# Performance work log

Measured on AMD Instinct MI355X. Metric: run time of the kernel, lower is better.

The kernel has to match this reference:

```python
import jax, jax.numpy as jnp
import numpy as np
import math

SQ, SK, B, NP, HN = 2048, 2048, 2, 16, 128
LAYER_NUM = 1  # coeff
NORM_FACTOR = math.sqrt(2048 / 16) * LAYER_NUM  # sqrt(HIDDEN/HEADS) * coeff
SCALE = float(LAYER_NUM)  # MLSASoftmax scale


def setup_inputs() -> dict:
    key = jax.random.key(0)
    kq, kk, kv = jax.random.split(key, 3)
    query_layer = jax.random.normal(kq, (SQ, B, NP, HN), dtype=jnp.float32)
    key_layer = jax.random.normal(kk, (SK, B, NP, HN), dtype=jnp.float32)
    value_layer = jax.random.normal(kv, (SK, B, NP, HN), dtype=jnp.float32)
    # Causal mask: True = masked, shape [b, 1, sq, sk] (broadcasts over heads)
    causal = jnp.triu(jnp.ones((SQ, SK), dtype=bool), k=1)
    attention_mask = jnp.broadcast_to(causal[None, None], (B, 1, SQ, SK))
    return {
        "query_layer": query_layer,
        "key_layer": key_layer,
        "value_layer": value_layer,
        "attention_mask": attention_mask,
    }


def reference(query_layer, key_layer, value_layer, attention_mask):
    # scores[b,n,s,t] = (Q . K) / norm_factor, then * coeff in softmax
    scores = jnp.einsum("sbnh,tbnh->bnst", query_layer, key_layer) / NORM_FACTOR
    scores = scores * SCALE
    scores = jnp.where(attention_mask, jnp.float32(-10000.0), scores)
    # Module computes exp/sum WITHOUT max-subtraction; replicate exactly.
    exp_mo = jnp.exp(scores)
    denomi = jnp.sum(exp_mo, axis=-1, keepdims=True)  # [b, np, sq, 1]
    probs = exp_mo / denomi
    # dropout is identity in eval / for deterministic baseline
    ctx = jnp.einsum("bnst,tbnh->sbnh", probs, value_layer)  # [sq, b, np, hn]
    sq, b, n, h = ctx.shape
    context_layer = ctx.reshape(sq, b, n * h)
    return (context_layer, denomi)
```

## Files before the change

### kernel.cpp

```cpp
#include <hip/hip_runtime.h>
#include <hip/hip_bf16.h>
#include <stdint.h>

typedef __attribute__((ext_vector_type(8))) short short8;
typedef __attribute__((ext_vector_type(8))) unsigned short ushort8;
typedef __attribute__((ext_vector_type(4))) float f32x4;
typedef __attribute__((ext_vector_type(4))) int int4v;

#define NHEAD 32
#define SEQ   2048
#define HN    128

static constexpr float INV_NORM = 0.08838834764831845f;

__device__ __forceinline__ unsigned short f2bf(float f) {
  union { float f; unsigned u; } v; v.f = f;
  unsigned r = v.u + 0x7fffu + ((v.u >> 16) & 1u);
  return (unsigned short)(r >> 16);
}

__device__ __forceinline__ f32x4 mfma16(short8 a, short8 b, f32x4 c) {
  return __builtin_amdgcn_mfma_f32_16x16x32_bf16(a, b, c, 0, 0, 0);
}

__device__ __forceinline__ void gl_lds16(const void* g, void* l) {
  __builtin_amdgcn_global_load_lds(
      (const __attribute__((address_space(1))) unsigned int*)g,
      (__attribute__((address_space(3))) unsigned int*)l, 16, 0, 0);
}

__global__ __launch_bounds__(256) void prep_kv(const float* __restrict__ K,
                                               const float* __restrict__ V,
                                               unsigned short* __restrict__ kswz,
                                               unsigned short* __restrict__ vT) {
  __shared__ unsigned short lds[128 * 136];
  int bid = blockIdx.x;
  int tid = threadIdx.x;
  if (bid < 4096) {
    int idx = bid * 256 + tid;
    int cl = idx & 15;
    int t  = (idx >> 4) & 2047;
    int bn = idx >> 15;
    const float4* src = (const float4*)(K + ((size_t)t * 32 + bn) * 128 + cl * 8);
    float4 a = src[0], b = src[1];
    ushort8 o;
    o[0]=f2bf(a.x); o[1]=f2bf(a.y); o[2]=f2bf(a.z); o[3]=f2bf(a.w);
    o[4]=f2bf(b.x); o[5]=f2bf(b.y); o[6]=f2bf(b.z); o[7]=f2bf(b.w);
    *(ushort8*)(kswz + ((size_t)bn * 2048 + t) * 128 + ((cl ^ (t & 7)) * 8)) = o;
  } else {
    int vb = bid - 4096;
    int bn = vb >> 4;
    int t0 = (vb & 15) << 7;
    int r = tid >> 1, h0 = (tid & 1) * 64;
    const float* src = V + ((size_t)(t0 + r) * 32 + bn) * 128 + h0;
#pragma unroll
    for (int j = 0; j < 8; ++j) {
      float4 a = *(const float4*)(src + j * 8);
      float4 b = *(const float4*)(src + j * 8 + 4);
      ushort8 o;
      o[0]=f2bf(a.x); o[1]=f2bf(a.y); o[2]=f2bf(a.z); o[3]=f2bf(a.w);
      o[4]=f2bf(b.x); o[5]=f2bf(b.y); o[6]=f2bf(b.z); o[7]=f2bf(b.w);
      *(ushort8*)&lds[r * 136 + h0 + j * 8] = o;
    }
    __syncthreads();
    int h = tid >> 1, ts = (tid & 1) * 64;
    unsigned short tmp[64];
#pragma unroll
    for (int j = 0; j < 64; ++j) {
      int p = j & 31;
      int tloc = ((p >> 3) & 3) * 4 + ((p >> 2) & 1) * 16 + (p & 3);
      tmp[j] = lds[(ts + (j & 32) + tloc) * 136 + h];
    }
    ushort8* dst = (ushort8*)(vT + ((size_t)bn * 128 + h) * 2048 + t0 + ts);
#pragma unroll
    for (int j = 0; j < 8; ++j) dst[j] = *(ushort8*)&tmp[j * 8];
  }
}

__device__ __forceinline__ void read_kf(const char* kb, int l15, int hi,
                                        short8 (&kf)[2][4]) {
  int xr = (l15 & 7) << 4;
#pragma unroll
  for (int nt = 0; nt < 2; ++nt) {
    const char* krow = kb + (nt * 16 + l15) * 256;
#pragma unroll
    for (int kk = 0; kk < 4; ++kk)
      kf[nt][kk] = *(const short8*)(krow + (((kk * 4 + hi) * 16) ^ xr));
  }
}

__device__ __forceinline__ void read_vf(const char* vbh, int l15, int hi,
                                        short8 (&vf)[8]) {
#pragma unroll
  for (int ht = 0; ht < 8; ++ht)
    vf[ht] = *(const short8*)(vbh + (ht * 16 + l15) * 64 +
                              ((((l15 >> 1) + hi) & 3) * 16));
}

__device__ __forceinline__ short8 packp(const float (&e)[8], float& da) {
  da += ((e[0] + e[1]) + (e[2] + e[3])) + ((e[4] + e[5]) + (e[6] + e[7]));
  unsigned w0, w1, w2, w3;
  asm("v_cvt_pk_bf16_f32 %0, %1, %2" : "=v"(w0) : "v"(e[0]), "v"(e[1]));
  asm("v_cvt_pk_bf16_f32 %0, %1, %2" : "=v"(w1) : "v"(e[2]), "v"(e[3]));
  asm("v_cvt_pk_bf16_f32 %0, %1, %2" : "=v"(w2) : "v"(e[4]), "v"(e[5]));
  asm("v_cvt_pk_bf16_f32 %0, %1, %2" : "=v"(w3) : "v"(e[6]), "v"(e[7]));
  union { int4v u; short8 s; } pk;
  pk.u = (int4v){(int)w0, (int)w1, (int)w2, (int)w3};
  return pk.s;
}

__device__ __forceinline__ short8 softp_m(const f32x4 (&sv)[2], int t0h, int qbase,
                                          int l15, int hi, float& da) {
  float e[8];
#pragma unroll
  for (int nt = 0; nt < 2; ++nt)
#pragma unroll
    for (int i = 0; i < 4; ++i) {
      float x = __expf(sv[nt][i]);
      int kv = t0h + nt * 16 + hi * 4 + i;
      e[nt * 4 + i] = (kv <= qbase + l15) ? x : 0.0f;
    }
  return packp(e, da);
}

__device__ __forceinline__ short8 softp_u(const f32x4 (&sv)[2], float& da) {
  float e[8];
#pragma unroll
  for (int nt = 0; nt < 2; ++nt)
#pragma unroll
    for (int i = 0; i < 4; ++i)
      e[nt * 4 + i] = __expf(sv[nt][i]);
  return packp(e, da);
}

__global__ __launch_bounds__(256, 2) void attn_main(const float* __restrict__ Q,
                                                    const unsigned short* __restrict__ kswz,
                                                    const unsigned short* __restrict__ vT,
                                                    float* __restrict__ out) {
  __shared__ char smem[32768];
  int tid = threadIdx.x;
  int lane = tid & 63;
  int w = tid >> 6;
  int l15 = lane & 15;
  int hi = lane >> 4;

  int bid = blockIdx.x;
  int bn = bid & 31;
  int z = bid >> 5;
  int g = z & 7, s = z >> 3;
  int qt = (s == 0) ? (31 - g) : (s == 1) ? (16 + g) : (s == 2) ? (15 - g) : g;
  int qb = qt * 64 + w * 16;
  int ntile = 2 * qt + 2;

  short8 qf[4];
  {
    const float* qrow = Q + ((size_t)(qb + l15) * 32 + bn) * 128;
#pragma unroll
    for (int kk = 0; kk < 4; ++kk) {
      float4 a = *(const float4*)(qrow + kk * 32 + hi * 8);
      float4 b = *(const float4*)(qrow + kk * 32 + hi * 8 + 4);
      short8 o;
      o[0]=(short)f2bf(a.x*INV_NORM); o[1]=(short)f2bf(a.y*INV_NORM);
      o[2]=(short)f2bf(a.z*INV_NORM); o[3]=(short)f2bf(a.w*INV_NORM);
      o[4]=(short)f2bf(b.x*INV_NORM); o[5]=(short)f2bf(b.y*INV_NORM);
      o[6]=(short)f2bf(b.z*INV_NORM); o[7]=(short)f2bf(b.w*INV_NORM);
      qf[kk] = o;
    }
  }

  f32x4 zz = {0.f, 0.f, 0.f, 0.f};
  f32x4 acc[8];
#pragma unroll
  for (int ht = 0; ht < 8; ++ht) acc[ht] = zz;
  float dacc = 0.f;

  const char* kg = (const char*)(kswz + (size_t)bn * 2048 * 128);
  const char* vg = (const char*)(vT + (size_t)bn * 128 * 2048);

  auto stage = [&](int buf, int t) {
    const char* ksrc = kg + (size_t)t * 8192;
    char* kl = smem + buf * 8192;
    int c = w * 64 + lane;
#pragma unroll
    for (int rr = 0; rr < 2; ++rr)
      gl_lds16(ksrc + (size_t)(c + rr * 256) * 16, kl + (c + rr * 256) * 16);
    char* vl = smem + 16384 + buf * 8192;
#pragma unroll
    for (int rr = 0; rr < 2; ++rr) {
      int c2 = c + rr * 256;
      int h = c2 >> 2, sp = c2 & 3;
      int sl = (sp - (h >> 1)) & 3;
      gl_lds16(vg + (size_t)h * 4096 + (size_t)t * 64 + sl * 16,
               vl + c2 * 16);
    }
  };

  asm volatile("s_waitcnt vmcnt(0)" ::: "memory");
  stage(0, 0);

  int cur = 0;
  for (int it = 0; it < ntile; ++it) {
    int t0h = it * 32;
    asm volatile("s_waitcnt vmcnt(0)" ::: "memory");
    __builtin_amdgcn_s_barrier();

    const char* kb = smem + cur * 8192;
    const char* vbh = smem + 16384 + cur * 8192;
    bool act = (t0h <= qb + 15);

    short8 kf[2][4];
    if (act) read_kf(kb, l15, hi, kf);
    if (it + 1 < ntile) stage(cur ^ 1, it + 1);

    if (act) {
      f32x4 sv[2] = {zz, zz};
      __builtin_amdgcn_s_setprio(1);
#pragma unroll
      for (int nt = 0; nt < 2; ++nt)
#pragma unroll
        for (int kk = 0; kk < 4; ++kk)
          sv[nt] = mfma16(kf[nt][kk], qf[kk], sv[nt]);
      __builtin_amdgcn_s_setprio(0);
      short8 vf[8];
      read_vf(vbh, l15, hi, vf);
      bool mask = (t0h + 31 > qb);
      short8 p = mask ? softp_m(sv, t0h, qb, l15, hi, dacc)
                      : softp_u(sv, dacc);
      __builtin_amdgcn_s_setprio(1);
#pragma unroll
      for (int ht = 0; ht < 8; ++ht)
        acc[ht] = mfma16(p, vf[ht], acc[ht]);
      __builtin_amdgcn_s_setprio(0);
    }
    cur ^= 1;
  }

  {
    float d = dacc;
    d += __shfl_xor(d, 16);
    d += __shfl_xor(d, 32);
    dacc = d;
  }
  float* dn = out + 8388608;
  if (hi == 0) dn[(size_t)bn * 2048 + qb + l15] = dacc;

  float inv[4];
#pragma unroll
  for (int i = 0; i < 4; ++i)
    inv[i] = __builtin_amdgcn_rcpf(__shfl(dacc, hi * 4 + i));

#pragma unroll
  for (int i = 0; i < 4; ++i) {
    float* orow = out + (size_t)(qb + hi * 4 + i) * 4096 + bn * 128 + l15;
#pragma unroll
    for (int ht = 0; ht < 8; ++ht)
      orow[ht * 16] = acc[ht][i] * inv[i];
  }
}

extern "C" void kernel_launch(void* const* d_in, const int* in_sizes, int n_in,
                              void* d_out, int out_size, void* d_ws, size_t ws_size,
                              hipStream_t stream) {
  const float* Q = (const float*)d_in[0];
  const float* K = (const float*)d_in[1];
  const float* V = (const float*)d_in[2];
  float* out = (float*)d_out;

  unsigned short* kswz = (unsigned short*)d_ws;
  unsigned short* vT   = kswz + (size_t)NHEAD * SEQ * HN;

  prep_kv<<<4608, 256, 0, stream>>>(K, V, kswz, vT);
  attn_main<<<1024, 256, 0, stream>>>(Q, kswz, vT, out);
}
```

Baseline: 85.30 us.

## Split KV loop across two wave groups per block and merge partial results

Doubles the block to 512 threads. Two groups of four waves each process alternating KV tiles with their own double-buffered LDS regions, then merge the partial accumulators and denominators through shared memory. The aim is to halve the serial KV loop length per block and expose more parallelism for the causal workload. The q-tile ordering is simplified to descending order. The cost is double the LDS (64KB), a shared-memory reduction epilogue, and likely lower occupancy.

```diff
diff --git a/kernel.cpp b/kernel.cpp
--- a/kernel.cpp
+++ b/kernel.cpp
@@ -133,24 +133,25 @@
   return packp(e, da);
 }
 
-__global__ __launch_bounds__(256, 2) void attn_main(const float* __restrict__ Q,
+__global__ __launch_bounds__(512, 2) void attn_main(const float* __restrict__ Q,
                                                     const unsigned short* __restrict__ kswz,
                                                     const unsigned short* __restrict__ vT,
                                                     float* __restrict__ out) {
-  __shared__ char smem[32768];
+  __shared__ char smem[65536];
   int tid = threadIdx.x;
   int lane = tid & 63;
-  int w = tid >> 6;
+  int w8 = tid >> 6;
+  int w = w8 & 3;
+  int sid = w8 >> 2;
   int l15 = lane & 15;
   int hi = lane >> 4;
 
   int bid = blockIdx.x;
   int bn = bid & 31;
   int z = bid >> 5;
-  int g = z & 7, s = z >> 3;
-  int qt = (s == 0) ? (31 - g) : (s == 1) ? (16 + g) : (s == 2) ? (15 - g) : g;
+  int qt = 31 - z;
   int qb = qt * 64 + w * 16;
-  int ntile = 2 * qt + 2;
+  int nIt = qt + 1;
 
   short8 qf[4];
   {
@@ -177,14 +178,17 @@
   const char* kg = (const char*)(kswz + (size_t)bn * 2048 * 128);
   const char* vg = (const char*)(vT + (size_t)bn * 128 * 2048);
 
+  char* kbase = smem + sid * 16384;
+  char* vbase = smem + 32768 + sid * 16384;
+
   auto stage = [&](int buf, int t) {
     const char* ksrc = kg + (size_t)t * 8192;
-    char* kl = smem + buf * 8192;
+    char* kl = kbase + buf * 8192;
     int c = w * 64 + lane;
 #pragma unroll
     for (int rr = 0; rr < 2; ++rr)
       gl_lds16(ksrc + (size_t)(c + rr * 256) * 16, kl + (c + rr * 256) * 16);
-    char* vl = smem + 16384 + buf * 8192;
+    char* vl = vbase + buf * 8192;
 #pragma unroll
     for (int rr = 0; rr < 2; ++rr) {
       int c2 = c + rr * 256;
@@ -196,21 +200,22 @@
   };
 
   asm volatile("s_waitcnt vmcnt(0)" ::: "memory");
-  stage(0, 0);
+  stage(0, sid);
 
   int cur = 0;
-  for (int it = 0; it < ntile; ++it) {
-    int t0h = it * 32;
+  for (int it = 0; it < nIt; ++it) {
+    int t = it * 2 + sid;
+    int t0h = t * 32;
     asm volatile("s_waitcnt vmcnt(0)" ::: "memory");
     __builtin_amdgcn_s_barrier();
 
-    const char* kb = smem + cur * 8192;
-    const char* vbh = smem + 16384 + cur * 8192;
+    const char* kb = kbase + cur * 8192;
+    const char* vbh = vbase + cur * 8192;
     bool act = (t0h <= qb + 15);
 
     short8 kf[2][4];
     if (act) read_kf(kb, l15, hi, kf);
-    if (it + 1 < ntile) stage(cur ^ 1, it + 1);
+    if (it + 1 < nIt) stage(cur ^ 1, t + 2);
 
     if (act) {
       f32x4 sv[2] = {zz, zz};
@@ -235,6 +240,27 @@
     cur ^= 1;
   }
 
+  __syncthreads();
+  int sl = w * 64 + lane;
+  float* dsm = (float*)smem;
+  if (sid == 1) dsm[sl] = dacc;
+  __syncthreads();
+  if (sid == 0) dacc += dsm[sl];
+  __syncthreads();
+  f32x4* accsm = (f32x4*)smem;
+  if (sid == 1) {
+#pragma unroll
+    for (int ht = 0; ht < 8; ++ht) accsm[ht * 256 + sl] = acc[ht];
+  }
+  __syncthreads();
+  if (sid == 1) return;
+#pragma unroll
+  for (int ht = 0; ht < 8; ++ht) {
+    f32x4 o = accsm[ht * 256 + sl];
+    acc[ht][0] += o[0]; acc[ht][1] += o[1];
+    acc[ht][2] += o[2]; acc[ht][3] += o[3];
+  }
+
   {
     float d = dacc;
     d += __shfl_xor(d, 16);
@@ -270,5 +296,5 @@
   unsigned short* vT   = kswz + (size_t)NHEAD * SEQ * HN;
 
   prep_kv<<<4608, 256, 0, stream>>>(K, V, kswz, vT);
-  attn_main<<<1024, 256, 0, stream>>>(Q, kswz, vT, out);
-}
+  attn_main<<<1024, 512, 0, stream>>>(Q, kswz, vT, out);
+}
```

New measurement: 93.65 us. 1.1x slower.

## Double block size to 8 waves and 128-row query tiles with 64-key stages

Applied to the files above, without the earlier changes.

Each block now runs 8 waves covering 128 query rows and stages 64 keys per iteration (two 32-key halves) into a doubled 64KB LDS double buffer. Each staged K/V tile is shared by twice as many waves, which halves global-to-LDS traffic per query and halves the number of barriers. The block schedule is simplified to a 16-tile reverse/forward ordering. In exchange the grid drops to 512 blocks, LDS use per block doubles, and causal load balancing is coarser because inactive waves still wait at each barrier.

```diff
diff --git a/kernel.cpp b/kernel.cpp
--- a/kernel.cpp
+++ b/kernel.cpp
@@ -133,11 +133,11 @@
   return packp(e, da);
 }
 
-__global__ __launch_bounds__(256, 2) void attn_main(const float* __restrict__ Q,
+__global__ __launch_bounds__(512, 2) void attn_main(const float* __restrict__ Q,
                                                     const unsigned short* __restrict__ kswz,
                                                     const unsigned short* __restrict__ vT,
                                                     float* __restrict__ out) {
-  __shared__ char smem[32768];
+  __shared__ char smem[65536];
   int tid = threadIdx.x;
   int lane = tid & 63;
   int w = tid >> 6;
@@ -147,9 +147,8 @@
   int bid = blockIdx.x;
   int bn = bid & 31;
   int z = bid >> 5;
-  int g = z & 7, s = z >> 3;
-  int qt = (s == 0) ? (31 - g) : (s == 1) ? (16 + g) : (s == 2) ? (15 - g) : g;
-  int qb = qt * 64 + w * 16;
+  int qt = (z < 8) ? (15 - z) : (z - 8);
+  int qb = qt * 128 + w * 16;
   int ntile = 2 * qt + 2;
 
   short8 qf[4];
@@ -177,21 +176,20 @@
   const char* kg = (const char*)(kswz + (size_t)bn * 2048 * 128);
   const char* vg = (const char*)(vT + (size_t)bn * 128 * 2048);
 
-  auto stage = [&](int buf, int t) {
-    const char* ksrc = kg + (size_t)t * 8192;
-    char* kl = smem + buf * 8192;
-    int c = w * 64 + lane;
+  auto stage = [&](int buf, int t0) {
+    const char* ksrc = kg + (size_t)t0 * 256;
+    char* kl = smem + buf * 16384;
+    int c = tid;
 #pragma unroll
     for (int rr = 0; rr < 2; ++rr)
-      gl_lds16(ksrc + (size_t)(c + rr * 256) * 16, kl + (c + rr * 256) * 16);
-    char* vl = smem + 16384 + buf * 8192;
-#pragma unroll
-    for (int rr = 0; rr < 2; ++rr) {
-      int c2 = c + rr * 256;
-      int h = c2 >> 2, sp = c2 & 3;
+      gl_lds16(ksrc + (size_t)(c + rr * 512) * 16, kl + (c + rr * 512) * 16);
+    char* vl = smem + 32768 + buf * 16384;
+#pragma unroll
+    for (int s = 0; s < 2; ++s) {
+      int h = c >> 2, sp = c & 3;
       int sl = (sp - (h >> 1)) & 3;
-      gl_lds16(vg + (size_t)h * 4096 + (size_t)t * 64 + sl * 16,
-               vl + c2 * 16);
+      gl_lds16(vg + (size_t)h * 4096 + (t0 + s * 32) * 2 + sl * 16,
+               vl + s * 8192 + c * 16);
     }
   };
 
@@ -200,37 +198,40 @@
 
   int cur = 0;
   for (int it = 0; it < ntile; ++it) {
-    int t0h = it * 32;
+    int t0 = it * 64;
     asm volatile("s_waitcnt vmcnt(0)" ::: "memory");
     __builtin_amdgcn_s_barrier();
-
-    const char* kb = smem + cur * 8192;
-    const char* vbh = smem + 16384 + cur * 8192;
-    bool act = (t0h <= qb + 15);
-
-    short8 kf[2][4];
-    if (act) read_kf(kb, l15, hi, kf);
-    if (it + 1 < ntile) stage(cur ^ 1, it + 1);
-
-    if (act) {
-      f32x4 sv[2] = {zz, zz};
-      __builtin_amdgcn_s_setprio(1);
-#pragma unroll
-      for (int nt = 0; nt < 2; ++nt)
-#pragma unroll
-        for (int kk = 0; kk < 4; ++kk)
-          sv[nt] = mfma16(kf[nt][kk], qf[kk], sv[nt]);
-      __builtin_amdgcn_s_setprio(0);
-      short8 vf[8];
-      read_vf(vbh, l15, hi, vf);
-      bool mask = (t0h + 31 > qb);
-      short8 p = mask ? softp_m(sv, t0h, qb, l15, hi, dacc)
-                      : softp_u(sv, dacc);
-      __builtin_amdgcn_s_setprio(1);
-#pragma unroll
-      for (int ht = 0; ht < 8; ++ht)
-        acc[ht] = mfma16(p, vf[ht], acc[ht]);
-      __builtin_amdgcn_s_setprio(0);
+    if (it + 1 < ntile) stage(cur ^ 1, t0 + 64);
+
+    const char* kb = smem + cur * 16384;
+    const char* vb = smem + 32768 + cur * 16384;
+#pragma unroll
+    for (int half = 0; half < 2; ++half) {
+      int t0h = t0 + half * 32;
+      if (t0h <= qb + 15) {
+        const char* kbh = kb + half * 8192;
+        const char* vbh = vb + half * 8192;
+        short8 kf[2][4];
+        read_kf(kbh, l15, hi, kf);
+        f32x4 sv[2] = {zz, zz};
+        __builtin_amdgcn_s_setprio(1);
+#pragma unroll
+        for (int nt = 0; nt < 2; ++nt)
+#pragma unroll
+          for (int kk = 0; kk < 4; ++kk)
+            sv[nt] = mfma16(kf[nt][kk], qf[kk], sv[nt]);
+        __builtin_amdgcn_s_setprio(0);
+        short8 vf[8];
+        read_vf(vbh, l15, hi, vf);
+        bool mask = (t0h + 31 > qb);
+        short8 p = mask ? softp_m(sv, t0h, qb, l15, hi, dacc)
+                        : softp_u(sv, dacc);
+        __builtin_amdgcn_s_setprio(1);
+#pragma unroll
+        for (int ht = 0; ht < 8; ++ht)
+          acc[ht] = mfma16(p, vf[ht], acc[ht]);
+        __builtin_amdgcn_s_setprio(0);
+      }
     }
     cur ^= 1;
   }
@@ -270,5 +271,5 @@
   unsigned short* vT   = kswz + (size_t)NHEAD * SEQ * HN;
 
   prep_kv<<<4608, 256, 0, stream>>>(K, V, kswz, vT);
-  attn_main<<<1024, 256, 0, stream>>>(Q, kswz, vT, out);
-}
+  attn_main<<<512, 512, 0, stream>>>(Q, kswz, vT, out);
+}
```

Measured after the change: 80.74 us. 5.3% less time.

## Pre-layout K/V in MFMA fragment order and load directly from global, dropping LDS staging

Applied to the files above, without the earlier changes.

The prep kernel now writes K and V in the exact per-lane MFMA fragment order, so the attention kernel can read each fragment with a coalesced 16-byte global load per lane. This removes the LDS double buffer, the global-to-LDS copies and the per-tile barriers, and lets each wave exit its loop independently once its causal range ends. The query-tile scheduling order is also changed. In exchange, K/V are re-read from L2 by every wave with no software prefetch, so memory latency is exposed more directly.

```diff
diff --git a/kernel.cpp b/kernel.cpp
--- a/kernel.cpp
+++ b/kernel.cpp
@@ -23,16 +23,10 @@
   return __builtin_amdgcn_mfma_f32_16x16x32_bf16(a, b, c, 0, 0, 0);
 }
 
-__device__ __forceinline__ void gl_lds16(const void* g, void* l) {
-  __builtin_amdgcn_global_load_lds(
-      (const __attribute__((address_space(1))) unsigned int*)g,
-      (__attribute__((address_space(3))) unsigned int*)l, 16, 0, 0);
-}
-
 __global__ __launch_bounds__(256) void prep_kv(const float* __restrict__ K,
                                                const float* __restrict__ V,
-                                               unsigned short* __restrict__ kswz,
-                                               unsigned short* __restrict__ vT) {
+                                               unsigned short* __restrict__ kfr,
+                                               unsigned short* __restrict__ vfr) {
   __shared__ unsigned short lds[128 * 136];
   int bid = blockIdx.x;
   int tid = threadIdx.x;
@@ -46,7 +40,11 @@
     ushort8 o;
     o[0]=f2bf(a.x); o[1]=f2bf(a.y); o[2]=f2bf(a.z); o[3]=f2bf(a.w);
     o[4]=f2bf(b.x); o[5]=f2bf(b.y); o[6]=f2bf(b.z); o[7]=f2bf(b.w);
-    *(ushort8*)(kswz + ((size_t)bn * 2048 + t) * 128 + ((cl ^ (t & 7)) * 8)) = o;
+    int tile = t >> 5, r = t & 31;
+    int nt = r >> 4, lr = r & 15;
+    int kk = cl >> 2, hc = cl & 3;
+    *(ushort8*)(kfr + (size_t)bn * 262144 + tile * 4096 +
+                (nt * 4 + kk) * 512 + (hc * 16 + lr) * 8) = o;
   } else {
     int vb = bid - 4096;
     int bn = vb >> 4;
@@ -71,30 +69,16 @@
       int tloc = ((p >> 3) & 3) * 4 + ((p >> 2) & 1) * 16 + (p & 3);
       tmp[j] = lds[(ts + (j & 32) + tloc) * 136 + h];
     }
-    ushort8* dst = (ushort8*)(vT + ((size_t)bn * 128 + h) * 2048 + t0 + ts);
-#pragma unroll
-    for (int j = 0; j < 8; ++j) dst[j] = *(ushort8*)&tmp[j * 8];
-  }
-}
-
-__device__ __forceinline__ void read_kf(const char* kb, int l15, int hi,
-                                        short8 (&kf)[2][4]) {
-  int xr = (l15 & 7) << 4;
-#pragma unroll
-  for (int nt = 0; nt < 2; ++nt) {
-    const char* krow = kb + (nt * 16 + l15) * 256;
-#pragma unroll
-    for (int kk = 0; kk < 4; ++kk)
-      kf[nt][kk] = *(const short8*)(krow + (((kk * 4 + hi) * 16) ^ xr));
-  }
-}
-
-__device__ __forceinline__ void read_vf(const char* vbh, int l15, int hi,
-                                        short8 (&vf)[8]) {
-#pragma unroll
-  for (int ht = 0; ht < 8; ++ht)
-    vf[ht] = *(const short8*)(vbh + (ht * 16 + l15) * 64 +
-                              ((((l15 >> 1) + hi) & 3) * 16));
+#pragma unroll
+    for (int j = 0; j < 8; ++j) {
+      int c0 = t0 + ts + j * 8;
+      int tg = c0 >> 5;
+      int hv = (c0 >> 3) & 3;
+      size_t du = (size_t)bn * 32768 + (size_t)tg * 512 +
+                  (h >> 4) * 64 + hv * 16 + (h & 15);
+      *(ushort8*)(vfr + du * 8) = *(ushort8*)&tmp[j * 8];
+    }
+  }
 }
 
 __device__ __forceinline__ short8 packp(const float (&e)[8], float& da) {
@@ -134,10 +118,9 @@
 }
 
 __global__ __launch_bounds__(256, 2) void attn_main(const float* __restrict__ Q,
-                                                    const unsigned short* __restrict__ kswz,
-                                                    const unsigned short* __restrict__ vT,
+                                                    const unsigned short* __restrict__ kfr,
+                                                    const unsigned short* __restrict__ vfr,
                                                     float* __restrict__ out) {
-  __shared__ char smem[32768];
   int tid = threadIdx.x;
   int lane = tid & 63;
   int w = tid >> 6;
@@ -147,8 +130,8 @@
   int bid = blockIdx.x;
   int bn = bid & 31;
   int z = bid >> 5;
-  int g = z & 7, s = z >> 3;
-  int qt = (s == 0) ? (31 - g) : (s == 1) ? (16 + g) : (s == 2) ? (15 - g) : g;
+  int qt = (z < 8) ? (31 - z) : (z < 16) ? (z - 8)
+                   : (z < 24) ? (39 - z) : (z - 16);
   int qb = qt * 64 + w * 16;
   int ntile = 2 * qt + 2;
 
@@ -174,65 +157,45 @@
   for (int ht = 0; ht < 8; ++ht) acc[ht] = zz;
   float dacc = 0.f;
 
-  const char* kg = (const char*)(kswz + (size_t)bn * 2048 * 128);
-  const char* vg = (const char*)(vT + (size_t)bn * 128 * 2048);
-
-  auto stage = [&](int buf, int t) {
-    const char* ksrc = kg + (size_t)t * 8192;
-    char* kl = smem + buf * 8192;
-    int c = w * 64 + lane;
-#pragma unroll
-    for (int rr = 0; rr < 2; ++rr)
-      gl_lds16(ksrc + (size_t)(c + rr * 256) * 16, kl + (c + rr * 256) * 16);
-    char* vl = smem + 16384 + buf * 8192;
-#pragma unroll
-    for (int rr = 0; rr < 2; ++rr) {
-      int c2 = c + rr * 256;
-      int h = c2 >> 2, sp = c2 & 3;
-      int sl = (sp - (h >> 1)) & 3;
-      gl_lds16(vg + (size_t)h * 4096 + (size_t)t * 64 + sl * 16,
-               vl + c2 * 16);
-    }
-  };
-
-  asm volatile("s_waitcnt vmcnt(0)" ::: "memory");
-  stage(0, 0);
-
-  int cur = 0;
+  const char* kg = (const char*)kfr + (size_t)bn * 524288;
+  const char* vg = (const char*)vfr + (size_t)bn * 524288;
+
   for (int it = 0; it < ntile; ++it) {
     int t0h = it * 32;
-    asm volatile("s_waitcnt vmcnt(0)" ::: "memory");
-    __builtin_amdgcn_s_barrier();
-
-    const char* kb = smem + cur * 8192;
-    const char* vbh = smem + 16384 + cur * 8192;
-    bool act = (t0h <= qb + 15);
+    if (t0h > qb + 15) break;
+    const char* kb = kg + (size_t)it * 8192;
+    const char* vb = vg + (size_t)it * 8192;
 
     short8 kf[2][4];
-    if (act) read_kf(kb, l15, hi, kf);
-    if (it + 1 < ntile) stage(cur ^ 1, it + 1);
-
-    if (act) {
-      f32x4 sv[2] = {zz, zz};
-      __builtin_amdgcn_s_setprio(1);
-#pragma unroll
-      for (int nt = 0; nt < 2; ++nt)
-#pragma unroll
-        for (int kk = 0; kk < 4; ++kk)
-          sv[nt] = mfma16(kf[nt][kk], qf[kk], sv[nt]);
-      __builtin_amdgcn_s_setprio(0);
-      short8 vf[8];
-      read_vf(vbh, l15, hi, vf);
-      bool mask = (t0h + 31 > qb);
-      short8 p = mask ? softp_m(sv, t0h, qb, l15, hi, dacc)
-                      : softp_u(sv, dacc);
-      __builtin_amdgcn_s_setprio(1);
-#pragma unroll
-      for (int ht = 0; ht < 8; ++ht)
-        acc[ht] = mfma16(p, vf[ht], acc[ht]);
-      __builtin_amdgcn_s_setprio(0);
-    }
-    cur ^= 1;
+#pragma unroll
+    for (int nt = 0; nt < 2; ++nt)
+#pragma unroll
+      for (int kk = 0; kk < 4; ++kk)
+        kf[nt][kk] = *(const short8*)(kb + (nt * 4 + kk) * 1024 + lane * 16);
+
+    f32x4 sv[2] = {zz, zz};
+    __builtin_amdgcn_s_setprio(1);
+#pragma unroll
+    for (int nt = 0; nt < 2; ++nt)
+#pragma unroll
+      for (int kk = 0; kk < 4; ++kk)
+        sv[nt] = mfma16(kf[nt][kk], qf[kk], sv[nt]);
+    __builtin_amdgcn_s_setprio(0);
+
+    short8 vf[8];
+#pragma unroll
+    for (int ht = 0; ht < 8; ++ht)
+      vf[ht] = *(const short8*)(vb + ht * 1024 + lane * 16);
+
+    bool mask = (t0h + 31 > qb);
+    short8 p = mask ? softp_m(sv, t0h, qb, l15, hi, dacc)
+                    : softp_u(sv, dacc);
+
+    __builtin_amdgcn_s_setprio(1);
+#pragma unroll
+    for (int ht = 0; ht < 8; ++ht)
+      acc[ht] = mfma16(p, vf[ht], acc[ht]);
+    __builtin_amdgcn_s_setprio(0);
   }
 
   {
@@ -266,9 +229,9 @@
   const float* V = (const float*)d_in[2];
   float* out = (float*)d_out;
 
-  unsigned short* kswz = (unsigned short*)d_ws;
-  unsigned short* vT   = kswz + (size_t)NHEAD * SEQ * HN;
-
-  prep_kv<<<4608, 256, 0, stream>>>(K, V, kswz, vT);
-  attn_main<<<1024, 256, 0, stream>>>(Q, kswz, vT, out);
-}
+  unsigned short* kfr = (unsigned short*)d_ws;
+  unsigned short* vfr = kfr + (size_t)NHEAD * SEQ * HN;
+
+  prep_kv<<<4608, 256, 0, stream>>>(K, V, kfr, vfr);
+  attn_main<<<1024, 256, 0, stream>>>(Q, kfr, vfr, out);
+}
```

Result: slower. 100.6 us (+18.0%).
